# Performance work log

Measured on AMD Instinct MI355X. Metric: run time of the kernel, lower is better.

Reference implementation:

```python
import jax, jax.numpy as jnp
import numpy as np
import math

B, T, C, H = 8, 1024, 1024, 16
D = C // H

def _layernorm(x, w, b, eps=1e-5):
    mean = jnp.mean(x, axis=-1, keepdims=True)
    var = jnp.var(x, axis=-1, keepdims=True)
    return (x - mean) / jnp.sqrt(var + eps) * w + b

def setup_inputs() -> dict:
    key = jax.random.key(0)
    ks = jax.random.split(key, 8)
    s = 0.02
    return {
        "x": jax.random.normal(ks[0], (B, T, C), dtype=jnp.float32),
        "Wqkv": jax.random.normal(ks[1], (C, 3 * C), dtype=jnp.float32) * s,
        "bqkv": jnp.zeros((3 * C,), dtype=jnp.float32),
        "Wo": jax.random.normal(ks[2], (C, C), dtype=jnp.float32) * s,
        "bo": jnp.zeros((C,), dtype=jnp.float32),
        "ln1_w": jnp.ones((C,), dtype=jnp.float32),
        "ln1_b": jnp.zeros((C,), dtype=jnp.float32),
        "ln2_w": jnp.ones((C,), dtype=jnp.float32),
        "ln2_b": jnp.zeros((C,), dtype=jnp.float32),
        "Wfc": jax.random.normal(ks[3], (C, 4 * C), dtype=jnp.float32) * s,
        "bfc": jnp.zeros((4 * C,), dtype=jnp.float32),
        "Wp": jax.random.normal(ks[4], (4 * C, C), dtype=jnp.float32) * s,
        "bp": jnp.zeros((C,), dtype=jnp.float32),
    }

def _block(x, Wqkv, bqkv, Wo, bo, ln1_w, ln1_b, ln2_w, ln2_b, Wfc, bfc, Wp, bp):
    # --- attention branch ---
    h = _layernorm(x, ln1_w, ln1_b)
    qkv = h @ Wqkv + bqkv                      # [B,T,3C]
    q, k, v = jnp.split(qkv, 3, axis=2)
    q = q.reshape(B, T, H, D)
    k = k.reshape(B, T, H, D)
    v = v.reshape(B, T, H, D)
    # NOTE: source scales by 1/sqrt(C) (full embed dim), faithful to original
    attn = jnp.einsum('bqhd,bkhd->bhqk', q, k) * (1.0 / math.sqrt(C))
    causal = jnp.tril(jnp.ones((T, T), dtype=bool))
    attn = jnp.where(causal[None, None], attn, -jnp.inf)
    attn = jax.nn.softmax(attn, axis=-1)
    y = jnp.einsum('bhqk,bkhd->bqhd', attn, v).reshape(B, T, C)
    y = y @ Wo + bo
    x = x + y
    # --- MLP branch ---
    h2 = _layernorm(x, ln2_w, ln2_b)
    m = jax.nn.gelu(h2 @ Wfc + bfc)            # approximate gelu (nnx default)
    m = m @ Wp + bp
    return x + m

def reference(x, Wqkv, bqkv, Wo, bo, ln1_w, ln1_b, ln2_w, ln2_b, Wfc, bfc, Wp, bp):
    return _block(x, Wqkv, bqkv, Wo, bo, ln1_w, ln1_b, ln2_w, ln2_b, Wfc, bfc, Wp, bp)
```

## Files before the change

kernel.cpp:

```cpp
#include <hip/hip_runtime.h>


typedef __bf16 bf16;
typedef bf16 bf16x8 __attribute__((ext_vector_type(8)));
typedef bf16 bf16x4 __attribute__((ext_vector_type(4)));
typedef float f32x4 __attribute__((ext_vector_type(4)));

#define GLOAD_LDS16(g, l)                                                      \
  __builtin_amdgcn_global_load_lds(                                            \
      (const __attribute__((address_space(1))) void*)(g),                      \
      (__attribute__((address_space(3))) void*)(l), 16, 0, 0)

#if __has_builtin(__builtin_amdgcn_exp2f)
#define EXP2F(x) __builtin_amdgcn_exp2f(x)
#else
#define EXP2F(x) exp2f(x)
#endif

static __device__ __forceinline__ f32x4 mfma16(bf16x8 a, bf16x8 b, f32x4 c) {
  return __builtin_amdgcn_mfma_f32_16x16x32_bf16(a, b, c, 0, 0, 0);
}

__global__ __launch_bounds__(256) void ln_kernel(const float* __restrict__ x,
                                                 const float* __restrict__ w,
                                                 const float* __restrict__ b,
                                                 bf16* __restrict__ out) {
  const int row = blockIdx.x;
  const int t = threadIdx.x;
  const float4 v = reinterpret_cast<const float4*>(x + (size_t)row * 1024)[t];
  float s = v.x + v.y + v.z + v.w;
  float s2 = v.x * v.x + v.y * v.y + v.z * v.z + v.w * v.w;
#pragma unroll
  for (int off = 32; off >= 1; off >>= 1) {
    s += __shfl_xor(s, off, 64);
    s2 += __shfl_xor(s2, off, 64);
  }
  __shared__ float red[8];
  if ((t & 63) == 0) {
    red[t >> 6] = s;
    red[4 + (t >> 6)] = s2;
  }
  __syncthreads();
  s = red[0] + red[1] + red[2] + red[3];
  s2 = red[4] + red[5] + red[6] + red[7];
  const float mean = s * (1.0f / 1024.0f);
  const float var = s2 * (1.0f / 1024.0f) - mean * mean;
  const float rstd = rsqrtf(var + 1e-5f);
  const float4 wv = reinterpret_cast<const float4*>(w)[t];
  const float4 bv = reinterpret_cast<const float4*>(b)[t];
  bf16x4 o;
  o[0] = (bf16)((v.x - mean) * rstd * wv.x + bv.x);
  o[1] = (bf16)((v.y - mean) * rstd * wv.y + bv.y);
  o[2] = (bf16)((v.z - mean) * rstd * wv.z + bv.z);
  o[3] = (bf16)((v.w - mean) * rstd * wv.w + bv.w);
  *reinterpret_cast<bf16x4*>(out + (size_t)row * 1024 + t * 4) = o;
}

__global__ __launch_bounds__(256) void transpose_cast_kernel(
    const float* __restrict__ W, bf16* __restrict__ Wt, int K, int N) {
  __shared__ float tile[64][65];
  const int c0 = blockIdx.x * 64;
  const int r0 = blockIdx.y * 64;
  const int t = threadIdx.x;
  const int tr = t >> 4;
  const int tc = (t & 15) * 4;
#pragma unroll
  for (int rr = 0; rr < 4; ++rr) {
    const int lr = rr * 16 + tr;
    const float4 v =
        *reinterpret_cast<const float4*>(&W[(size_t)(r0 + lr) * N + c0 + tc]);
    tile[lr][tc] = v.x;
    tile[lr][tc + 1] = v.y;
    tile[lr][tc + 2] = v.z;
    tile[lr][tc + 3] = v.w;
  }
  __syncthreads();
#pragma unroll
  for (int rr = 0; rr < 4; ++rr) {
    const int ln = rr * 16 + tr;
    bf16x4 o;
#pragma unroll
    for (int i = 0; i < 4; ++i) o[i] = (bf16)tile[tc + i][ln];
    *reinterpret_cast<bf16x4*>(&Wt[(size_t)(c0 + ln) * K + r0 + tc]) = o;
  }
}

template <int EPI>
__global__ __launch_bounds__(256) void gemm_kernel(
    const bf16* __restrict__ A, const bf16* __restrict__ Bt,
    const float* __restrict__ bias, const float* resid, float* outf,
    bf16* __restrict__ outb, int Ndim, int Kdim) {
  __shared__ __align__(16) bf16 As[128 * 64];
  __shared__ __align__(16) bf16 Bs[128 * 64];
  const int t = threadIdx.x;
  const int l = t & 63;
  const int w = t >> 6;
  const int lg = l >> 4, lc = l & 15;
  const int wr = w >> 1, wc = w & 1;

  const int gx = gridDim.x;
  const int nwg = gx * gridDim.y;
  int flat = blockIdx.x + blockIdx.y * gx;
  if ((nwg & 7) == 0) {
    const int ch = nwg >> 3;
    flat = (flat & 7) * ch + (flat >> 3);
  }
  const int m0 = (flat / gx) * 128;
  const int n0 = (flat % gx) * 128;

  f32x4 acc[4][4];
#pragma unroll
  for (int m = 0; m < 4; ++m)
#pragma unroll
    for (int n = 0; n < 4; ++n) acc[m][n] = {0.f, 0.f, 0.f, 0.f};

  const int sr = t >> 3;
  const int sc = (t & 7) * 8;

  for (int k0 = 0; k0 < Kdim; k0 += 64) {
    __syncthreads();
#pragma unroll
    for (int j = 0; j < 4; ++j) {
      const int row = j * 32 + sr;
      const int col = sc ^ ((row & 7) * 8);
      GLOAD_LDS16(A + (size_t)(m0 + row) * Kdim + k0 + col,
                  &As[j * 2048 + t * 8]);
    }
#pragma unroll
    for (int j = 0; j < 4; ++j) {
      const int row = j * 32 + sr;
      const int col = sc ^ ((row & 7) * 8);
      GLOAD_LDS16(Bt + (size_t)(n0 + row) * Kdim + k0 + col,
                  &Bs[j * 2048 + t * 8]);
    }
    __syncthreads();
#pragma unroll
    for (int ks = 0; ks < 2; ++ks) {
      bf16x8 af[4], bfr[4];
#pragma unroll
      for (int m = 0; m < 4; ++m) {
        const int row = wr * 64 + m * 16 + lc;
        af[m] = *reinterpret_cast<const bf16x8*>(
            &As[row * 64 + ((ks * 32 + 8 * lg) ^ ((row & 7) * 8))]);
      }
#pragma unroll
      for (int n = 0; n < 4; ++n) {
        const int row = wc * 64 + n * 16 + lc;
        bfr[n] = *reinterpret_cast<const bf16x8*>(
            &Bs[row * 64 + ((ks * 32 + 8 * lg) ^ ((row & 7) * 8))]);
      }
#pragma unroll
      for (int m = 0; m < 4; ++m)
#pragma unroll
        for (int n = 0; n < 4; ++n) acc[m][n] = mfma16(af[m], bfr[n], acc[m][n]);
    }
  }

#pragma unroll
  for (int n = 0; n < 4; ++n) {
    const int col = n0 + wc * 64 + n * 16 + lc;
    const float bv = bias[col];
#pragma unroll
    for (int m = 0; m < 4; ++m) {
      const int row0 = m0 + wr * 64 + m * 16 + lg * 4;
#pragma unroll
      for (int r = 0; r < 4; ++r) {
        const size_t idx = (size_t)(row0 + r) * Ndim + col;
        const float v = acc[m][n][r] + bv;
        if (EPI == 0) {
          outb[idx] = (bf16)v;
        } else if (EPI == 1) {
          const float g =
              0.5f * v *
              (1.0f + tanhf(0.79788456080286535588f * (v + 0.044715f * v * v * v)));
          outb[idx] = (bf16)g;
        } else {
          outf[idx] = v + resid[idx];
        }
      }
    }
  }
}

__global__ __launch_bounds__(256) void attn_kernel(const bf16* __restrict__ qkv,
                                                   bf16* __restrict__ y) {
  const int flat = blockIdx.x + (blockIdx.y << 3) + (blockIdx.z << 7);
  const int swz = (flat & 7) * 128 + (flat >> 3);
  const int qt = swz & 7;
  const int h = (swz >> 3) & 15;
  const int b = swz >> 7;
  const int qb0 = qt * 128;

  const int t = threadIdx.x;
  const int l = t & 63;
  const int w = t >> 6;
  const int lg = l >> 4, lc = l & 15;

  __shared__ __align__(16) bf16 QPs[128 * 64];
  __shared__ __align__(16) bf16 Ksm[2][64 * 64];
  __shared__ __align__(16) bf16 Vtm[2][64 * 64];

  const size_t base = (size_t)b * 1024 * 3072;
  const int sr = t >> 3;
  const int sc = (t & 7) * 8;
  const int vd0 = (t & 31) * 2;
  const int vk0 = (t >> 5) * 8;

#pragma unroll
  for (int j = 0; j < 4; ++j) {
    const int row = j * 32 + sr;
    const int col = sc ^ ((row & 7) * 8);
    GLOAD_LDS16(qkv + base + (size_t)(qb0 + row) * 3072 + h * 64 + col,
                &QPs[j * 2048 + t * 8]);
  }
#pragma unroll
  for (int j = 0; j < 2; ++j) {
    const int row = j * 32 + sr;
    const int col = sc ^ ((row & 7) * 8);
    GLOAD_LDS16(qkv + base + (size_t)row * 3072 + 1024 + h * 64 + col,
                &Ksm[0][j * 2048 + t * 8]);
  }
  unsigned int v8[8];
#pragma unroll
  for (int i = 0; i < 8; ++i)
    v8[i] = *reinterpret_cast<const unsigned int*>(
        qkv + base + (size_t)(vk0 + i) * 3072 + 2048 + h * 64 + vd0);
  __syncthreads();

  bf16x8 qf[2][2];
#pragma unroll
  for (int mf = 0; mf < 2; ++mf)
#pragma unroll
    for (int ks = 0; ks < 2; ++ks) {
      const int row = w * 32 + mf * 16 + lc;
      qf[mf][ks] = *reinterpret_cast<const bf16x8*>(
          &QPs[row * 64 + ((ks * 32 + 8 * lg) ^ ((row & 7) * 8))]);
    }
  {
    bf16x8 wlo, whi;
#pragma unroll
    for (int i = 0; i < 8; ++i) {
      wlo[i] = __builtin_bit_cast(bf16, (unsigned short)(v8[i] & 0xffffu));
      whi[i] = __builtin_bit_cast(bf16, (unsigned short)(v8[i] >> 16));
    }
    *reinterpret_cast<bf16x8*>(&Vtm[0][vd0 * 64 + (vk0 ^ ((vd0 & 7) * 8))]) = wlo;
    *reinterpret_cast<bf16x8*>(
        &Vtm[0][(vd0 + 1) * 64 + (vk0 ^ (((vd0 + 1) & 7) * 8))]) = whi;
  }
  __syncthreads();

  bf16* const Pw = &QPs[w * 2048];

  const float KS = 0.04508422f;
  const float THR = 177.0f;

  float mrow[2][4], mK[2][4], lsum[2][4];
  f32x4 oacc[2][4];
#pragma unroll
  for (int mf = 0; mf < 2; ++mf)
#pragma unroll
    for (int r = 0; r < 4; ++r) {
      mrow[mf][r] = -1e30f;
      mK[mf][r] = 0.f;
      lsum[mf][r] = 0.f;
    }
#pragma unroll
  for (int mf = 0; mf < 2; ++mf)
#pragma unroll
    for (int nd = 0; nd < 4; ++nd) oacc[mf][nd] = {0.f, 0.f, 0.f, 0.f};

  const int nkv = qt * 2 + 2;
  for (int kt = 0; kt < nkv; ++kt) {
    const int cur = kt & 1, nxt = cur ^ 1;
    const int kv0t = kt << 6;
    const bool hasnext = (kt + 1 < nkv);

    if (hasnext) {
      const int kn = (kt + 1) << 6;
#pragma unroll
      for (int j = 0; j < 2; ++j) {
        const int row = j * 32 + sr;
        const int col = sc ^ ((row & 7) * 8);
        GLOAD_LDS16(qkv + base + (size_t)(kn + row) * 3072 + 1024 + h * 64 + col,
                    &Ksm[nxt][j * 2048 + t * 8]);
      }
#pragma unroll
      for (int i = 0; i < 8; ++i)
        v8[i] = *reinterpret_cast<const unsigned int*>(
            qkv + base + (size_t)(kn + vk0 + i) * 3072 + 2048 + h * 64 + vd0);
    }

    f32x4 s[2][4];
#pragma unroll
    for (int mf = 0; mf < 2; ++mf)
#pragma unroll
      for (int nf = 0; nf < 4; ++nf) s[mf][nf] = {0.f, 0.f, 0.f, 0.f};
#pragma unroll
    for (int ks = 0; ks < 2; ++ks) {
      bf16x8 kf[4];
#pragma unroll
      for (int nf = 0; nf < 4; ++nf) {
        const int row = nf * 16 + lc;
        kf[nf] = *reinterpret_cast<const bf16x8*>(
            &Ksm[cur][row * 64 + ((ks * 32 + 8 * lg) ^ ((row & 7) * 8))]);
      }
#pragma unroll
      for (int mf = 0; mf < 2; ++mf)
#pragma unroll
        for (int nf = 0; nf < 4; ++nf)
          s[mf][nf] = mfma16(qf[mf][ks], kf[nf], s[mf][nf]);
    }

    if (kv0t + 63 > qb0 + w * 32) {
#pragma unroll
      for (int mf = 0; mf < 2; ++mf)
#pragma unroll
        for (int nf = 0; nf < 4; ++nf) {
          const int kg = kv0t + nf * 16 + lc;
#pragma unroll
          for (int r = 0; r < 4; ++r) {
            const int qg = qb0 + w * 32 + mf * 16 + lg * 4 + r;
            if (kg > qg) s[mf][nf][r] = -1e30f;
          }
        }
    }

    float lm[2][4];
    bool ok = true;
#pragma unroll
    for (int mf = 0; mf < 2; ++mf)
#pragma unroll
      for (int r = 0; r < 4; ++r) {
        lm[mf][r] = fmaxf(fmaxf(s[mf][0][r], s[mf][1][r]),
                          fmaxf(s[mf][2][r], s[mf][3][r]));
        ok = ok && (lm[mf][r] <= mrow[mf][r] + THR);
      }
    if (!__all(ok)) {
#pragma unroll
      for (int mf = 0; mf < 2; ++mf)
#pragma unroll
        for (int r = 0; r < 4; ++r) {
          float pm = lm[mf][r];
#pragma unroll
          for (int off = 8; off >= 1; off >>= 1)
            pm = fmaxf(pm, __shfl_xor(pm, off, 64));
          const float mnew = fmaxf(mrow[mf][r], pm);
          const float a = EXP2F((mrow[mf][r] - mnew) * KS);
          mrow[mf][r] = mnew;
          mK[mf][r] = mnew * KS;
          lsum[mf][r] *= a;
#pragma unroll
          for (int nd = 0; nd < 4; ++nd) oacc[mf][nd][r] *= a;
        }
    }

#pragma unroll
    for (int mf = 0; mf < 2; ++mf)
#pragma unroll
      for (int r = 0; r < 4; ++r) {
        const int pr = mf * 16 + lg * 4 + r;
        float acc = 0.f;
#pragma unroll
        for (int nf = 0; nf < 4; ++nf) {
          const float p = EXP2F(__builtin_fmaf(s[mf][nf][r], KS, -mK[mf][r]));
          acc += p;
          Pw[pr * 64 + ((nf * 16 + lc) ^ ((pr & 7) * 8))] = (bf16)p;
        }
        lsum[mf][r] += acc;
      }

    if (hasnext) {
      bf16x8 wlo, whi;
#pragma unroll
      for (int i = 0; i < 8; ++i) {
        wlo[i] = __builtin_bit_cast(bf16, (unsigned short)(v8[i] & 0xffffu));
        whi[i] = __builtin_bit_cast(bf16, (unsigned short)(v8[i] >> 16));
      }
      *reinterpret_cast<bf16x8*>(
          &Vtm[nxt][vd0 * 64 + (vk0 ^ ((vd0 & 7) * 8))]) = wlo;
      *reinterpret_cast<bf16x8*>(
          &Vtm[nxt][(vd0 + 1) * 64 + (vk0 ^ (((vd0 + 1) & 7) * 8))]) = whi;
    }

#pragma unroll
    for (int ks = 0; ks < 2; ++ks) {
      bf16x8 pf[2], vf[4];
#pragma unroll
      for (int mf = 0; mf < 2; ++mf) {
        const int row = mf * 16 + lc;
        pf[mf] = *reinterpret_cast<const bf16x8*>(
            &Pw[row * 64 + ((ks * 32 + 8 * lg) ^ ((row & 7) * 8))]);
      }
#pragma unroll
      for (int nd = 0; nd < 4; ++nd) {
        const int row = nd * 16 + lc;
        vf[nd] = *reinterpret_cast<const bf16x8*>(
            &Vtm[cur][row * 64 + ((ks * 32 + 8 * lg) ^ ((row & 7) * 8))]);
      }
#pragma unroll
      for (int mf = 0; mf < 2; ++mf)
#pragma unroll
        for (int nd = 0; nd < 4; ++nd)
          oacc[mf][nd] = mfma16(pf[mf], vf[nd], oacc[mf][nd]);
    }
    __syncthreads();
  }

#pragma unroll
  for (int mf = 0; mf < 2; ++mf)
#pragma unroll
    for (int r = 0; r < 4; ++r) {
      float ls = lsum[mf][r];
#pragma unroll
      for (int off = 8; off >= 1; off >>= 1) ls += __shfl_xor(ls, off, 64);
      lsum[mf][r] = 1.0f / ls;
    }
  const size_t ybase = (size_t)b * 1024 * 1024;
#pragma unroll
  for (int mf = 0; mf < 2; ++mf)
#pragma unroll
    for (int nd = 0; nd < 4; ++nd)
#pragma unroll
      for (int r = 0; r < 4; ++r) {
        const int qg = qb0 + w * 32 + mf * 16 + lg * 4 + r;
        const int d = nd * 16 + lc;
        y[ybase + (size_t)qg * 1024 + h * 64 + d] =
            (bf16)(oacc[mf][nd][r] * lsum[mf][r]);
      }
}

extern "C" void kernel_launch(void* const* d_in, const int* in_sizes, int n_in,
                              void* d_out, int out_size, void* d_ws,
                              size_t ws_size, hipStream_t stream) {
  (void)in_sizes; (void)n_in; (void)out_size; (void)ws_size;
  const float* x    = (const float*)d_in[0];
  const float* Wqkv = (const float*)d_in[1];
  const float* bqkv = (const float*)d_in[2];
  const float* Wo   = (const float*)d_in[3];
  const float* bo   = (const float*)d_in[4];
  const float* ln1w = (const float*)d_in[5];
  const float* ln1b = (const float*)d_in[6];
  const float* ln2w = (const float*)d_in[7];
  const float* ln2b = (const float*)d_in[8];
  const float* Wfc  = (const float*)d_in[9];
  const float* bfc  = (const float*)d_in[10];
  const float* Wp   = (const float*)d_in[11];
  const float* bp   = (const float*)d_in[12];
  float* out = (float*)d_out;
  char* ws = (char*)d_ws;

  bf16* WqkvT = (bf16*)(ws + 0);
  bf16* WoT   = (bf16*)(ws + 6291456);
  bf16* WfcT  = (bf16*)(ws + 8388608);
  bf16* WpT   = (bf16*)(ws + 16777216);
  bf16* h1    = (bf16*)(ws + 25165824);
  bf16* qkv   = (bf16*)(ws + 41943040);
  bf16* yb    = (bf16*)(ws + 92274688);
  bf16* fc    = (bf16*)(ws + 41943040);
  float* x1   = out;

  transpose_cast_kernel<<<dim3(48, 16), 256, 0, stream>>>(Wqkv, WqkvT, 1024, 3072);
  transpose_cast_kernel<<<dim3(16, 16), 256, 0, stream>>>(Wo, WoT, 1024, 1024);
  transpose_cast_kernel<<<dim3(64, 16), 256, 0, stream>>>(Wfc, WfcT, 1024, 4096);
  transpose_cast_kernel<<<dim3(16, 64), 256, 0, stream>>>(Wp, WpT, 4096, 1024);

  ln_kernel<<<8192, 256, 0, stream>>>(x, ln1w, ln1b, h1);
  gemm_kernel<0><<<dim3(24, 64), 256, 0, stream>>>(h1, WqkvT, bqkv, nullptr,
                                                   nullptr, qkv, 3072, 1024);
  attn_kernel<<<dim3(8, 16, 8), 256, 0, stream>>>(qkv, yb);
  gemm_kernel<2><<<dim3(8, 64), 256, 0, stream>>>(yb, WoT, bo, x, x1, nullptr,
                                                  1024, 1024);
  ln_kernel<<<8192, 256, 0, stream>>>(x1, ln2w, ln2b, h1);
  gemm_kernel<1><<<dim3(32, 64), 256, 0, stream>>>(h1, WfcT, bfc, nullptr,
                                                   nullptr, fc, 4096, 1024);
  gemm_kernel<2><<<dim3(8, 64), 256, 0, stream>>>(fc, WpT, bp, x1, out, nullptr,
                                                  1024, 4096);
}
```

Measured before the change: 525.8 us.

## Replace GEMM with 256-row tiles, 8 waves, double-buffered LDS pipeline

Swaps the 128x128 single-buffered GEMM for a 256xBN tile kernel with 512 threads and double-buffered LDS. Next-tile global-to-LDS loads are split into quarters and interleaved with MFMA phases, synchronised with explicit vmcnt waits, barriers and raised wave priority during MFMA. The GELU epilogue uses an exp2 and fast reciprocal instead of tanhf. In exchange it needs much more LDS and registers per block, and the larger tiles give fewer blocks for the N=1024 GEMMs, which can leave compute units underused.

```diff
diff --git a/kernel.cpp b/kernel.cpp
--- a/kernel.cpp
+++ b/kernel.cpp
@@ -10,12 +10,23 @@
   __builtin_amdgcn_global_load_lds(                                            \
       (const __attribute__((address_space(1))) void*)(g),                      \
       (__attribute__((address_space(3))) void*)(l), 16, 0, 0)
+
+#define S_VMCNT(n) asm volatile("s_waitcnt vmcnt(" #n ")" ::: "memory")
+#define S_BAR() __builtin_amdgcn_s_barrier()
 
 #if __has_builtin(__builtin_amdgcn_exp2f)
 #define EXP2F(x) __builtin_amdgcn_exp2f(x)
 #else
 #define EXP2F(x) exp2f(x)
 #endif
+
+static __device__ __forceinline__ float fast_rcp(float x) {
+#if __has_builtin(__builtin_amdgcn_rcpf)
+  return __builtin_amdgcn_rcpf(x);
+#else
+  return 1.0f / x;
+#endif
+}
 
 static __device__ __forceinline__ f32x4 mfma16(bf16x8 a, bf16x8 b, f32x4 c) {
   return __builtin_amdgcn_mfma_f32_16x16x32_bf16(a, b, c, 0, 0, 0);
@@ -85,18 +96,22 @@
   }
 }
 
-template <int EPI>
-__global__ __launch_bounds__(256) void gemm_kernel(
+template <int BN, int EPI>
+__global__ __launch_bounds__(512, 2) void gemm256_kernel(
     const bf16* __restrict__ A, const bf16* __restrict__ Bt,
-    const float* __restrict__ bias, const float* resid, float* outf,
-    bf16* __restrict__ outb, int Ndim, int Kdim) {
-  __shared__ __align__(16) bf16 As[128 * 64];
-  __shared__ __align__(16) bf16 Bs[128 * 64];
+    const float* __restrict__ bias, const float* __restrict__ resid,
+    float* __restrict__ outf, bf16* __restrict__ outb, int Ndim, int Kdim) {
+  constexpr int NB = BN / 128;
+  constexpr int LB = BN / 128;
+  __shared__ __align__(16) bf16 As[2][256 * 64];
+  __shared__ __align__(16) bf16 Bs[2][BN * 64];
+
   const int t = threadIdx.x;
   const int l = t & 63;
   const int w = t >> 6;
   const int lg = l >> 4, lc = l & 15;
-  const int wr = w >> 1, wc = w & 1;
+  const int wr = w >> 2;
+  const int wc = w & 3;
 
   const int gx = gridDim.x;
   const int nwg = gx * gridDim.y;
@@ -105,81 +120,137 @@
     const int ch = nwg >> 3;
     flat = (flat & 7) * ch + (flat >> 3);
   }
-  const int m0 = (flat / gx) * 128;
-  const int n0 = (flat % gx) * 128;
-
-  f32x4 acc[4][4];
-#pragma unroll
-  for (int m = 0; m < 4; ++m)
-#pragma unroll
-    for (int n = 0; n < 4; ++n) acc[m][n] = {0.f, 0.f, 0.f, 0.f};
+  const int m0 = (flat / gx) * 256;
+  const int n0 = (flat % gx) * BN;
 
   const int sr = t >> 3;
   const int sc = (t & 7) * 8;
-
-  for (int k0 = 0; k0 < Kdim; k0 += 64) {
-    __syncthreads();
-#pragma unroll
-    for (int j = 0; j < 4; ++j) {
-      const int row = j * 32 + sr;
-      const int col = sc ^ ((row & 7) * 8);
-      GLOAD_LDS16(A + (size_t)(m0 + row) * Kdim + k0 + col,
-                  &As[j * 2048 + t * 8]);
-    }
-#pragma unroll
-    for (int j = 0; j < 4; ++j) {
-      const int row = j * 32 + sr;
-      const int col = sc ^ ((row & 7) * 8);
-      GLOAD_LDS16(Bt + (size_t)(n0 + row) * Kdim + k0 + col,
-                  &Bs[j * 2048 + t * 8]);
-    }
-    __syncthreads();
-#pragma unroll
-    for (int ks = 0; ks < 2; ++ks) {
-      bf16x8 af[4], bfr[4];
-#pragma unroll
-      for (int m = 0; m < 4; ++m) {
-        const int row = wr * 64 + m * 16 + lc;
-        af[m] = *reinterpret_cast<const bf16x8*>(
-            &As[row * 64 + ((ks * 32 + 8 * lg) ^ ((row & 7) * 8))]);
-      }
-#pragma unroll
-      for (int n = 0; n < 4; ++n) {
-        const int row = wc * 64 + n * 16 + lc;
-        bfr[n] = *reinterpret_cast<const bf16x8*>(
-            &Bs[row * 64 + ((ks * 32 + 8 * lg) ^ ((row & 7) * 8))]);
-      }
+  const int scsw = sc ^ ((sr & 7) * 8);
+
+  f32x4 acc[2][2][4][NB];
+#pragma unroll
+  for (int mh = 0; mh < 2; ++mh)
+#pragma unroll
+    for (int nh = 0; nh < 2; ++nh)
 #pragma unroll
       for (int m = 0; m < 4; ++m)
 #pragma unroll
-        for (int n = 0; n < 4; ++n) acc[m][n] = mfma16(af[m], bfr[n], acc[m][n]);
-    }
-  }
-
-#pragma unroll
-  for (int n = 0; n < 4; ++n) {
-    const int col = n0 + wc * 64 + n * 16 + lc;
-    const float bv = bias[col];
+        for (int n = 0; n < NB; ++n) acc[mh][nh][m][n] = {0.f, 0.f, 0.f, 0.f};
+
+  bf16x8 af[4][2], bfr[NB][2];
+
+  auto stageA = [&](int buf, int half, int kcol) {
+#pragma unroll
+    for (int j = 0; j < 2; ++j) {
+      const int row = m0 + half * 128 + j * 64 + sr;
+      GLOAD_LDS16(A + (size_t)row * Kdim + kcol + scsw,
+                  &As[buf][half * 8192 + j * 4096 + t * 8]);
+    }
+  };
+  auto stageB = [&](int buf, int half, int kcol) {
+#pragma unroll
+    for (int j = 0; j < LB; ++j) {
+      const int row = n0 + half * (BN / 2) + j * 64 + sr;
+      GLOAD_LDS16(Bt + (size_t)row * Kdim + kcol + scsw,
+                  &Bs[buf][half * (BN / 2) * 64 + j * 4096 + t * 8]);
+    }
+  };
+  auto readA = [&](int buf, int mh) {
 #pragma unroll
     for (int m = 0; m < 4; ++m) {
-      const int row0 = m0 + wr * 64 + m * 16 + lg * 4;
-#pragma unroll
-      for (int r = 0; r < 4; ++r) {
-        const size_t idx = (size_t)(row0 + r) * Ndim + col;
-        const float v = acc[m][n][r] + bv;
-        if (EPI == 0) {
-          outb[idx] = (bf16)v;
-        } else if (EPI == 1) {
-          const float g =
-              0.5f * v *
-              (1.0f + tanhf(0.79788456080286535588f * (v + 0.044715f * v * v * v)));
-          outb[idx] = (bf16)g;
-        } else {
-          outf[idx] = v + resid[idx];
+      const int row = mh * 128 + wr * 64 + m * 16 + lc;
+#pragma unroll
+      for (int ks = 0; ks < 2; ++ks)
+        af[m][ks] = *reinterpret_cast<const bf16x8*>(
+            &As[buf][row * 64 + ((ks * 32 + 8 * lg) ^ ((row & 7) * 8))]);
+    }
+  };
+  auto readB = [&](int buf, int nh) {
+#pragma unroll
+    for (int n = 0; n < NB; ++n) {
+      const int row = nh * (BN / 2) + wc * (BN / 8) + n * 16 + lc;
+#pragma unroll
+      for (int ks = 0; ks < 2; ++ks)
+        bfr[n][ks] = *reinterpret_cast<const bf16x8*>(
+            &Bs[buf][row * 64 + ((ks * 32 + 8 * lg) ^ ((row & 7) * 8))]);
+    }
+  };
+  auto domfma = [&](int mh, int nh) {
+    __builtin_amdgcn_s_setprio(1);
+#pragma unroll
+    for (int ks = 0; ks < 2; ++ks)
+#pragma unroll
+      for (int m = 0; m < 4; ++m)
+#pragma unroll
+        for (int n = 0; n < NB; ++n)
+          acc[mh][nh][m][n] = mfma16(af[m][ks], bfr[n][ks], acc[mh][nh][m][n]);
+    __builtin_amdgcn_s_setprio(0);
+  };
+
+  const int NT = Kdim >> 6;
+
+  stageA(0, 0, 0);
+  stageA(0, 1, 0);
+  stageB(0, 0, 0);
+  stageB(0, 1, 0);
+  S_VMCNT(0);
+  S_BAR();
+
+  int cur = 0;
+  for (int kt = 0; kt < NT; ++kt) {
+    const int nxt = cur ^ 1;
+    const int kn = (kt + 1 < NT ? kt + 1 : kt) << 6;
+    readA(cur, 0);
+    readB(cur, 0);
+    stageA(nxt, 0, kn);
+    S_VMCNT(4);
+    S_BAR();
+    domfma(0, 0);
+    readB(cur, 1);
+    stageB(nxt, 0, kn);
+    if constexpr (BN == 256) S_VMCNT(4); else S_VMCNT(3);
+    S_BAR();
+    domfma(0, 1);
+    readA(cur, 1);
+    stageB(nxt, 1, kn);
+    if constexpr (BN == 256) S_VMCNT(4); else S_VMCNT(2);
+    S_BAR();
+    domfma(1, 1);
+    readB(cur, 0);
+    stageA(nxt, 1, kn);
+    if constexpr (BN == 256) S_VMCNT(4); else S_VMCNT(3);
+    S_BAR();
+    domfma(1, 0);
+    cur = nxt;
+  }
+
+#pragma unroll
+  for (int mh = 0; mh < 2; ++mh)
+#pragma unroll
+    for (int nh = 0; nh < 2; ++nh)
+#pragma unroll
+      for (int n = 0; n < NB; ++n) {
+        const int col = n0 + nh * (BN / 2) + wc * (BN / 8) + n * 16 + lc;
+        const float bv = bias[col];
+#pragma unroll
+        for (int m = 0; m < 4; ++m) {
+          const int row0 = m0 + mh * 128 + wr * 64 + m * 16 + lg * 4;
+#pragma unroll
+          for (int r = 0; r < 4; ++r) {
+            const size_t idx = (size_t)(row0 + r) * Ndim + col;
+            const float v = acc[mh][nh][m][n][r] + bv;
+            if (EPI == 0) {
+              outb[idx] = (bf16)v;
+            } else if (EPI == 1) {
+              const float e2 =
+                  EXP2F(-2.3022074f * (v + 0.044715f * v * v * v));
+              outb[idx] = (bf16)(v * fast_rcp(1.0f + e2));
+            } else {
+              outf[idx] = v + resid[idx];
+            }
+          }
         }
       }
-    }
-  }
 }
 
 __global__ __launch_bounds__(256) void attn_kernel(const bf16* __restrict__ qkv,
@@ -359,14 +430,14 @@
 #pragma unroll
       for (int r = 0; r < 4; ++r) {
         const int pr = mf * 16 + lg * 4 + r;
-        float acc = 0.f;
+        float accp = 0.f;
 #pragma unroll
         for (int nf = 0; nf < 4; ++nf) {
           const float p = EXP2F(__builtin_fmaf(s[mf][nf][r], KS, -mK[mf][r]));
-          acc += p;
+          accp += p;
           Pw[pr * 64 + ((nf * 16 + lc) ^ ((pr & 7) * 8))] = (bf16)p;
         }
-        lsum[mf][r] += acc;
+        lsum[mf][r] += accp;
       }
 
     if (hasnext) {
@@ -465,14 +536,14 @@
   transpose_cast_kernel<<<dim3(16, 64), 256, 0, stream>>>(Wp, WpT, 4096, 1024);
 
   ln_kernel<<<8192, 256, 0, stream>>>(x, ln1w, ln1b, h1);
-  gemm_kernel<0><<<dim3(24, 64), 256, 0, stream>>>(h1, WqkvT, bqkv, nullptr,
-                                                   nullptr, qkv, 3072, 1024);
+  gemm256_kernel<256, 0><<<dim3(12, 32), 512, 0, stream>>>(
+      h1, WqkvT, bqkv, nullptr, nullptr, qkv, 3072, 1024);
   attn_kernel<<<dim3(8, 16, 8), 256, 0, stream>>>(qkv, yb);
-  gemm_kernel<2><<<dim3(8, 64), 256, 0, stream>>>(yb, WoT, bo, x, x1, nullptr,
-                                                  1024, 1024);
+  gemm256_kernel<128, 2><<<dim3(8, 32), 512, 0, stream>>>(
+      yb, WoT, bo, x, x1, nullptr, 1024, 1024);
   ln_kernel<<<8192, 256, 0, stream>>>(x1, ln2w, ln2b, h1);
-  gemm_kernel<1><<<dim3(32, 64), 256, 0, stream>>>(h1, WfcT, bfc, nullptr,
-                                                   nullptr, fc, 4096, 1024);
-  gemm_kernel<2><<<dim3(8, 64), 256, 0, stream>>>(fc, WpT, bp, x1, out, nullptr,
-                                                  1024, 4096);
-}
+  gemm256_kernel<256, 1><<<dim3(16, 32), 512, 0, stream>>>(
+      h1, WfcT, bfc, nullptr, nullptr, fc, 4096, 1024);
+  gemm256_kernel<128, 2><<<dim3(8, 32), 512, 0, stream>>>(
+      fc, WpT, bp, x1, out, nullptr, 1024, 4096);
+}
```

Result: faster. 497.2 us (-5.4%).
